# Performance work log

Hardware: AMD Instinct MI355X
Metric: run time of the kernel (lower is better)

The kernel has to match this reference:

```python
import jax, jax.numpy as jnp
import numpy as np

D_NUM, P_NUM, LAYER, EMB = 1500, 4500, 3, 128


def _xavier(k, shape):
    lim = float(np.sqrt(6.0 / (shape[0] + shape[1])))
    return jax.random.uniform(k, shape, minval=-lim, maxval=lim, dtype=jnp.float32)


def _sym_norm(adj):
    # D^{-1/2} A D^{-1/2}, zero-degree safe (utils._create_*_adj_mat)
    deg = adj.sum(axis=1)
    dinv = jnp.where(deg > 0, jax.lax.rsqrt(jnp.maximum(deg, 1e-12)), 0.0)
    return adj * dinv[:, None] * dinv[None, :]


def _gcn(adj, emb, num):
    # LightGCN-style propagation: mean of layer-0..num embeddings (utils._gcn)
    def step(e, _):
        e = adj @ e
        return e, e
    _, layers = jax.lax.scan(step, emb, None, length=num)
    return (emb + layers.sum(axis=0)) / (num + 1)


def _neighbor_mean(mat, feats):
    # vectorized form of the per-row python loop: mean of feats over j where mat[i,j]==1, zeros if no neighbor
    m = (mat == 1.0).astype(feats.dtype)
    cnt = m.sum(axis=1, keepdims=True)
    return jnp.where(cnt > 0, (m @ feats) / jnp.maximum(cnt, 1.0), 0.0)


def _get_weight(emb, WA, BA, HA):
    return jax.nn.log_softmax(jax.nn.relu(emb @ WA + BA) @ HA, axis=0)


def setup_inputs():
    k = jax.random.split(jax.random.key(0), 24)
    N = D_NUM + P_NUM
    A = (jax.random.uniform(k[0], (5, N, N)) < 0.005).astype(jnp.float32)
    z = lambda: jnp.zeros((EMB,), jnp.float32)
    h = lambda: jnp.full((EMB, 1), 0.01, jnp.float32)
    return {
        "A": A,
        "drug_structure": jax.random.normal(k[1], (D_NUM, 160), jnp.float32),
        "protein_structure": jax.random.normal(k[2], (P_NUM, 512), jnp.float32),
        "lin_drug_w": _xavier(k[3], (160, EMB)), "lin_drug_b": z(),
        "lin_pro_w": _xavier(k[4], (512, EMB)), "lin_pro_b": z(),
        "p_weight": _xavier(k[5], (EMB, EMB)),
        "d_weight_i": _xavier(k[6], (EMB, EMB)),
        "pd_weight_p": _xavier(k[7], (EMB, EMB)),
        "pd_weight_d": _xavier(k[8], (EMB, EMB)),
        "dp_weight_p": _xavier(k[9], (EMB, EMB)),
        "WA_drug": _xavier(k[10], (EMB, EMB)), "BA_drug": z(), "HA_drug": h(),
        "WB_drug": _xavier(k[11], (EMB, EMB)), "BB_drug": z(), "HB_drug": h(),
        "WA_pro": _xavier(k[12], (EMB, EMB)), "BA_pro": z(), "HA_pro": h(),
        "WB_pro": _xavier(k[13], (EMB, EMB)), "BB_pro": z(), "HB_pro": h(),
        "WA_sim": _xavier(k[14], (EMB, EMB)), "BA_sim": z(), "HA_sim": h(),
        "layer": LAYER,
    }


def reference(A, drug_structure, protein_structure, lin_drug_w, lin_drug_b, lin_pro_w, lin_pro_b,
              p_weight, d_weight_i, pd_weight_p, pd_weight_d, dp_weight_p,
              WA_drug, BA_drug, HA_drug, WB_drug, BB_drug, HB_drug,
              WA_pro, BA_pro, HA_pro, WB_pro, BB_pro, HB_pro,
              WA_sim, BA_sim, HA_sim, layer):
    D, P = D_NUM, P_NUM
    R = A[0, :D, D:D + P]                       # drug-protein relation [D,P]
    dru_str = drug_structure @ lin_drug_w + lin_drug_b      # [D,128]
    pro_str = protein_structure @ lin_pro_w + lin_pro_b     # [P,128]

    def rel_emb(mat, feats, w):
        nei = _neighbor_mean(mat, feats)
        adj = _sym_norm((mat == 1.0).astype(feats.dtype))
        return _gcn(adj, feats @ w, layer), nei

    dru_rel_emb, dru_rel_nei = rel_emb(A[2, :D, :D], dru_str, d_weight_i)
    pro_rel_emb, pro_rel_nei = rel_emb(A[3, D:, D:], pro_str, p_weight)
    dru_sim_emb, dru_sim_nei = rel_emb(A[4, :D, :D], dru_str, d_weight_i)

    dru_tem = _neighbor_mean(R, pro_rel_nei)    # [D,128]
    # NB: torch 'dru_rel_nei + dru_sim_nei' concatenates python LISTS, and only
    # indices < D are ever read, so pro_tem effectively uses dru_rel_nei only.
    pro_tem = _neighbor_mean(R.T, dru_rel_nei)  # [P,128]

    # bipartite symmetric-normalized adjacency [[0,R],[R^T,0]]
    bip = jnp.zeros((D + P, D + P), R.dtype)
    bip = bip.at[:D, D:].set(R).at[D:, :D].set(R.T)
    adj = _sym_norm(bip)

    one_all = 0.8 * dru_str + 0.2 * dru_tem
    two_all = 0.8 * pro_str + 0.2 * pro_tem
    one_emb = dru_str @ pd_weight_d
    two_all = (two_all @ dp_weight_p) @ pd_weight_d
    two_emb = pro_str @ pd_weight_p
    dru_int = _gcn(adj, jnp.concatenate([one_emb, two_all], axis=0), layer)[:D]
    pro_int = _gcn(adj, jnp.concatenate([one_all, two_emb], axis=0), layer)[D:]

    drug_w = _get_weight(dru_int, WA_drug, BA_drug, HA_drug)
    pro_w = _get_weight(pro_int, WA_pro, BA_pro, HA_pro)
    dru_rel_w = _get_weight(dru_rel_emb, WB_drug, BB_drug, HB_drug)
    pro_rel_w = _get_weight(pro_rel_emb, WB_pro, BB_pro, HB_pro)
    dru_sim_w = _get_weight(dru_sim_emb, WA_sim, BA_sim, HA_sim)

    # faithful to source (including its asymmetric renormalization); dropout is eval-mode identity
    a_w = drug_w / (drug_w + dru_rel_w + dru_sim_w)
    b_w = dru_rel_w / (a_w + dru_rel_w + dru_sim_w)
    c_w = 1.0 - a_w - b_w
    fin_dru = a_w * dru_int + b_w * dru_rel_emb + c_w * dru_sim_emb

    pa = pro_w / (pro_w + pro_rel_w)
    pb = 1.0 - pa
    fin_pro = pa * pro_int + pb * pro_rel_emb

    y = fin_dru @ fin_pro.T                     # [D,P]
    y = (y - y.mean()) / jnp.std(y, ddof=1)     # torch.std is unbiased
    return jax.nn.sigmoid(y)
```

## Files before the change

kernel.cpp:

```cpp
#include <hip/hip_runtime.h>

constexpr int CAP = 128;
constexpr int RS_INV = 1, RS_RSQRT = 2, CS_RSQRT = 4, FINALIZE = 8;

struct BuildSeg { const float* M; long ldm; int rows; int cols; int col_off;
                  int* idx; int* cnt; };
struct LinJob  { const float* X; const float* X2; float pa, pb; int rows; int K;
                 const float* W; const float* bias; float* out; float* out2; };
struct SpmmJob { const int* idx; const int* cnt; int rows; int mod;
                 const float* X; float* out; float* acc; const float* init;
                 float* fin; int flags; };
struct AttnJob { const float* X; int rows; const float* W; const float* B;
                 const float* H; float* s; };

enum { SEG_ZERO = 0, SEG_B0 = 1, SEG_B1, SEG_B2, SEG_B3, SEG_SCAT = 5,
       SEG_SP0 = 6, SEG_SP1 = 7, SEG_LIN0 = 8, SEG_LIN1, SEG_LIN2, SEG_LIN3,
       SEG_AT0 = 12, SEG_AT1, SEG_AT2, SEG_SM0 = 15, SEG_SM1, SEG_SM2,
       NSEG = 18 };

struct Stage {
    int e[NSEG];
    int nZero; int* zeroPtr; double* stats;
    BuildSeg bs[4];
    int scatterTop; int* sIdx; int* sCnt;
    SpmmJob sp[2];
    LinJob lin[4];
    AttnJob at[3];
    float* smv[3]; int smn[3];
};

union SharedU {
    float Ws[32 * 128];
    float red[256];
};


__device__ __forceinline__ void build_unit(const BuildSeg& s, int lb)
{
    int row = lb * 4 + (threadIdx.x >> 6);
    if (row >= s.rows) return;
    int lane = threadIdx.x & 63;
    const float4* p4 = (const float4*)(s.M + (long)row * s.ldm);
    int* ri = s.idx + (long)row * CAP;
    int nv = s.cols >> 2;
    unsigned long long below = (1ULL << lane) - 1ULL;
    if (lane == 63) below = 0x7fffffffffffffffULL;
    int base = 0;
    for (int j0 = 0; j0 < nv; j0 += 64) {
        int jj = j0 + lane;
        float4 v = make_float4(0.f, 0.f, 0.f, 0.f);
        if (jj < nv) v = p4[jj];
        unsigned long long m0 = __ballot(v.x == 1.0f);
        unsigned long long m1 = __ballot(v.y == 1.0f);
        unsigned long long m2 = __ballot(v.z == 1.0f);
        unsigned long long m3 = __ballot(v.w == 1.0f);
        int pre = (int)(__popcll(m0 & below) + __popcll(m1 & below)
                      + __popcll(m2 & below) + __popcll(m3 & below));
        int o = base + pre;
        int cbase = (jj << 2) + s.col_off;
        if (v.x == 1.0f) { if (o < CAP) ri[o] = cbase;     ++o; }
        if (v.y == 1.0f) { if (o < CAP) ri[o] = cbase + 1; ++o; }
        if (v.z == 1.0f) { if (o < CAP) ri[o] = cbase + 2; ++o; }
        if (v.w == 1.0f) { if (o < CAP) ri[o] = cbase + 3; ++o; }
        base += (int)(__popcll(m0) + __popcll(m1) + __popcll(m2) + __popcll(m3));
    }
    if (lane == 0) s.cnt[row] = base < CAP ? base : CAP;
}

__device__ __forceinline__ void scatter_unit(int* idx, int* cnt, int topRows, int lb)
{
    int row = lb * 4 + (threadIdx.x >> 6);
    if (row >= topRows) return;
    int lane = threadIdx.x & 63;
    int n = cnt[row];
    const int* ri = idx + (long)row * CAP;
    for (int k = lane; k < n; k += 64) {
        int j = ri[k];
        int pos = atomicAdd(&cnt[j], 1);
        if (pos < CAP) idx[(long)j * CAP + pos] = row;
    }
}

__device__ __forceinline__ void spmm_tile(const SpmmJob& j, int lb)
{
    int c4 = threadIdx.x & 31;
    int row = lb * 8 + (threadIdx.x >> 5);
    if (row >= j.rows) return;
    int r_loc = row, xoff = 0;
    if (row >= j.mod) { r_loc = row - j.mod; xoff = j.mod; }
    int n = j.cnt[r_loc];
    const int* ri = j.idx + (long)r_loc * CAP;
    const float4* X4 = (const float4*)j.X;
    const bool csq = (j.flags & CS_RSQRT) != 0;
    float ax = 0.f, ay = 0.f, az = 0.f, aw = 0.f;
    int k = 0;
    for (; k + 2 <= n; k += 2) {
        int c0 = ri[k], c1 = ri[k + 1];
        float4 x0 = X4[(long)(c0 + xoff) * 32 + c4];
        float4 x1 = X4[(long)(c1 + xoff) * 32 + c4];
        float s0 = 1.0f, s1 = 1.0f;
        if (csq) {
            int n0 = j.cnt[c0], n1 = j.cnt[c1];
            s0 = (n0 > 0) ? rsqrtf((float)n0) : 0.0f;
            s1 = (n1 > 0) ? rsqrtf((float)n1) : 0.0f;
        }
        ax += x0.x * s0 + x1.x * s1;
        ay += x0.y * s0 + x1.y * s1;
        az += x0.z * s0 + x1.z * s1;
        aw += x0.w * s0 + x1.w * s1;
    }
    if (k < n) {
        int c0 = ri[k];
        float4 x0 = X4[(long)(c0 + xoff) * 32 + c4];
        float s0 = 1.0f;
        if (csq) {
            int n0 = j.cnt[c0];
            s0 = (n0 > 0) ? rsqrtf((float)n0) : 0.0f;
        }
        ax += x0.x * s0; ay += x0.y * s0; az += x0.z * s0; aw += x0.w * s0;
    }
    float rs = 1.0f;
    if (j.flags & RS_INV)        rs = (n > 0) ? 1.0f / (float)n : 0.0f;
    else if (j.flags & RS_RSQRT) rs = (n > 0) ? rsqrtf((float)n) : 0.0f;
    float4 v = make_float4(ax * rs, ay * rs, az * rs, aw * rs);
    long o = (long)row * 32 + c4;
    if (j.flags & FINALIZE) {
        float4 acc = ((const float4*)j.acc)[o];
        ((float4*)j.fin)[o] = make_float4((acc.x + v.x) * 0.25f, (acc.y + v.y) * 0.25f,
                                          (acc.z + v.z) * 0.25f, (acc.w + v.w) * 0.25f);
    } else {
        ((float4*)j.out)[o] = v;
        if (j.acc) {
            float4 base = j.init ? ((const float4*)j.init)[o] : ((const float4*)j.acc)[o];
            ((float4*)j.acc)[o] = make_float4(base.x + v.x, base.y + v.y,
                                              base.z + v.z, base.w + v.w);
        }
    }
}

__device__ void lin_tile(const LinJob& j, int lb, float* Ws)
{
    int c = threadIdx.x & 127;
    int row = lb * 2 + (threadIdx.x >> 7);
    if (j.W == nullptr) {
        if (row < j.rows) {
            long o = (long)row * 128 + c;
            float v = j.pa * j.X[o] + j.pb * j.X2[o];
            j.out[o] = v;
            if (j.out2) j.out2[o] = v;
        }
        return;
    }
    float acc = 0.0f;
    for (int k0 = 0; k0 < j.K; k0 += 32) {
        int chunk = min(32, j.K - k0);
        for (int e = threadIdx.x; e < chunk * 128; e += 256)
            Ws[e] = j.W[(long)(k0 + (e >> 7)) * 128 + (e & 127)];
        __syncthreads();
        if (row < j.rows) {
            const float* xr = j.X + (long)row * j.K + k0;
            const float* x2r = j.X2 ? j.X2 + (long)row * j.K + k0 : nullptr;
            #pragma unroll 4
            for (int kk = 0; kk < chunk; ++kk) {
                float v = xr[kk];
                if (j.X2) v = j.pa * v + j.pb * x2r[kk];
                acc += v * Ws[kk * 128 + c];
            }
        }
        __syncthreads();
    }
    if (row < j.rows) {
        float v = acc + (j.bias ? j.bias[c] : 0.0f);
        j.out[(long)row * 128 + c] = v;
        if (j.out2) j.out2[(long)row * 128 + c] = v;
    }
}

__device__ void attn_tile(const AttnJob& j, int lb, float* Ws)
{
    __shared__ float part[4];
    int c = threadIdx.x & 127;
    int row = lb * 2 + (threadIdx.x >> 7);
    float acc = 0.0f;
    for (int k0 = 0; k0 < 128; k0 += 32) {
        for (int e = threadIdx.x; e < 32 * 128; e += 256)
            Ws[e] = j.W[(long)(k0 + (e >> 7)) * 128 + (e & 127)];
        __syncthreads();
        if (row < j.rows) {
            const float* xr = j.X + (long)row * 128 + k0;
            #pragma unroll 4
            for (int kk = 0; kk < 32; ++kk)
                acc += xr[kk] * Ws[kk * 128 + c];
        }
        __syncthreads();
    }
    float v = 0.0f;
    if (row < j.rows) v = fmaxf(acc + j.B[c], 0.0f) * j.H[c];
    for (int o = 32; o > 0; o >>= 1) v += __shfl_down(v, o, 64);
    if ((threadIdx.x & 63) == 0) part[threadIdx.x >> 6] = v;
    __syncthreads();
    if (threadIdx.x == 0 && row < j.rows)   j.s[row] = part[0] + part[1];
    if (threadIdx.x == 128 && row < j.rows) j.s[row] = part[2] + part[3];
}

__device__ void softmax_vec(float* s, int n, float* red)
{
    int t = threadIdx.x;
    float m = -3.4e38f;
    for (int i = t; i < n; i += 256) m = fmaxf(m, s[i]);
    red[t] = m; __syncthreads();
    for (int o = 128; o > 0; o >>= 1) {
        if (t < o) red[t] = fmaxf(red[t], red[t + o]);
        __syncthreads();
    }
    m = red[0];
    __syncthreads();
    float sum = 0.0f;
    for (int i = t; i < n; i += 256) sum += expf(s[i] - m);
    red[t] = sum; __syncthreads();
    for (int o = 128; o > 0; o >>= 1) {
        if (t < o) red[t] += red[t + o];
        __syncthreads();
    }
    float lse = m + logf(red[0]);
    for (int i = t; i < n; i += 256) s[i] -= lse;
}

__global__ __launch_bounds__(256)
void k_stage(Stage s)
{
    __shared__ SharedU sh;
    int b = blockIdx.x;
    if (b < s.e[SEG_ZERO]) {
        int i = b * 256 + threadIdx.x;
        if (i < s.nZero) s.zeroPtr[i] = 0;
        if (b == 0 && threadIdx.x < 2 && s.stats) s.stats[threadIdx.x] = 0.0;
        return;
    }
    if (b < s.e[SEG_B0]) { build_unit(s.bs[0], b - s.e[SEG_B0 - 1]); return; }
    if (b < s.e[SEG_B1]) { build_unit(s.bs[1], b - s.e[SEG_B1 - 1]); return; }
    if (b < s.e[SEG_B2]) { build_unit(s.bs[2], b - s.e[SEG_B2 - 1]); return; }
    if (b < s.e[SEG_B3]) { build_unit(s.bs[3], b - s.e[SEG_B3 - 1]); return; }
    if (b < s.e[SEG_SCAT]) { scatter_unit(s.sIdx, s.sCnt, s.scatterTop, b - s.e[SEG_SCAT - 1]); return; }
    if (b < s.e[SEG_SP0]) { spmm_tile(s.sp[0], b - s.e[SEG_SP0 - 1]); return; }
    if (b < s.e[SEG_SP1]) { spmm_tile(s.sp[1], b - s.e[SEG_SP1 - 1]); return; }
    if (b < s.e[SEG_LIN0]) { lin_tile(s.lin[0], b - s.e[SEG_LIN0 - 1], sh.Ws); return; }
    if (b < s.e[SEG_LIN1]) { lin_tile(s.lin[1], b - s.e[SEG_LIN1 - 1], sh.Ws); return; }
    if (b < s.e[SEG_LIN2]) { lin_tile(s.lin[2], b - s.e[SEG_LIN2 - 1], sh.Ws); return; }
    if (b < s.e[SEG_LIN3]) { lin_tile(s.lin[3], b - s.e[SEG_LIN3 - 1], sh.Ws); return; }
    if (b < s.e[SEG_AT0]) { attn_tile(s.at[0], b - s.e[SEG_AT0 - 1], sh.Ws); return; }
    if (b < s.e[SEG_AT1]) { attn_tile(s.at[1], b - s.e[SEG_AT1 - 1], sh.Ws); return; }
    if (b < s.e[SEG_AT2]) { attn_tile(s.at[2], b - s.e[SEG_AT2 - 1], sh.Ws); return; }
    if (b < s.e[SEG_SM0]) { softmax_vec(s.smv[0], s.smn[0], sh.red); return; }
    if (b < s.e[SEG_SM1]) { softmax_vec(s.smv[1], s.smn[1], sh.red); return; }
    if (b < s.e[SEG_SM2]) { softmax_vec(s.smv[2], s.smn[2], sh.red); return; }
}

__global__ void k_fin(const float* __restrict__ wd, const float* __restrict__ wdr,
                      const float* __restrict__ wds,
                      const float4* __restrict__ ei, const float4* __restrict__ er,
                      const float4* __restrict__ es,
                      const float* __restrict__ wp, const float* __restrict__ wpr,
                      const float4* __restrict__ pi, const float4* __restrict__ pr,
                      float4* __restrict__ fd, float4* __restrict__ fp,
                      long nD4, long tot4)
{
    long i = (long)blockIdx.x * 256 + threadIdx.x;
    if (i >= tot4) return;
    if (i < nD4) {
        int r = (int)(i >> 5);
        float aL = wd[r], bL = wdr[r], cL = wds[r];
        float x = aL / (aL + bL + cL);
        float y = bL / (x + bL + cL);
        float z = 1.0f - x - y;
        float4 a = ei[i], b = er[i], c = es[i];
        fd[i] = make_float4(x * a.x + y * b.x + z * c.x, x * a.y + y * b.y + z * c.y,
                            x * a.z + y * b.z + z * c.z, x * a.w + y * b.w + z * c.w);
    } else {
        long k = i - nD4;
        int r = (int)(k >> 5);
        float pa = wp[r] / (wp[r] + wpr[r]);
        float pb = 1.0f - pa;
        float4 a = pi[k], b = pr[k];
        fp[k] = make_float4(pa * a.x + pb * b.x, pa * a.y + pb * b.y,
                            pa * a.z + pb * b.z, pa * a.w + pb * b.w);
    }
}

__global__ __launch_bounds__(256)
void k_ygemm(const float* __restrict__ Af, const float* __restrict__ Bf,
             int M, int N, float* __restrict__ y, double* __restrict__ stats)
{
    __shared__ float Ast[32][65];
    __shared__ float Bst[32][65];
    __shared__ double r1[256];
    __shared__ double r2[256];
    int i0 = blockIdx.y * 64, j0 = blockIdx.x * 64;
    int tx = threadIdx.x & 15, ty = threadIdx.x >> 4;
    float acc[4][4] = {};
    for (int k0 = 0; k0 < 128; k0 += 32) {
        for (int e = threadIdx.x; e < 64 * 32; e += 256) {
            int r = e >> 5, kk = e & 31;
            int ia = i0 + r, jb = j0 + r;
            Ast[kk][r] = (ia < M) ? Af[(long)ia * 128 + k0 + kk] : 0.0f;
            Bst[kk][r] = (jb < N) ? Bf[(long)jb * 128 + k0 + kk] : 0.0f;
        }
        __syncthreads();
        #pragma unroll 8
        for (int kk = 0; kk < 32; ++kk) {
            float a0 = Ast[kk][ty];      float a1 = Ast[kk][ty + 16];
            float a2 = Ast[kk][ty + 32]; float a3 = Ast[kk][ty + 48];
            float b0 = Bst[kk][tx];      float b1 = Bst[kk][tx + 16];
            float b2 = Bst[kk][tx + 32]; float b3 = Bst[kk][tx + 48];
            acc[0][0] += a0 * b0; acc[0][1] += a0 * b1; acc[0][2] += a0 * b2; acc[0][3] += a0 * b3;
            acc[1][0] += a1 * b0; acc[1][1] += a1 * b1; acc[1][2] += a1 * b2; acc[1][3] += a1 * b3;
            acc[2][0] += a2 * b0; acc[2][1] += a2 * b1; acc[2][2] += a2 * b2; acc[2][3] += a2 * b3;
            acc[3][0] += a3 * b0; acc[3][1] += a3 * b1; acc[3][2] += a3 * b2; acc[3][3] += a3 * b3;
        }
        __syncthreads();
    }
    double s1 = 0.0, s2 = 0.0;
    #pragma unroll
    for (int q = 0; q < 4; ++q) {
        int i = i0 + ty + 16 * q;
        if (i < M) {
            #pragma unroll
            for (int p = 0; p < 4; ++p) {
                int j = j0 + tx + 16 * p;
                if (j < N) {
                    float v = acc[q][p];
                    y[(long)i * N + j] = v;
                    s1 += v; s2 += (double)v * v;
                }
            }
        }
    }
    r1[threadIdx.x] = s1; r2[threadIdx.x] = s2;
    __syncthreads();
    for (int o = 128; o > 0; o >>= 1) {
        if (threadIdx.x < o) {
            r1[threadIdx.x] += r1[threadIdx.x + o];
            r2[threadIdx.x] += r2[threadIdx.x + o];
        }
        __syncthreads();
    }
    if (threadIdx.x == 0) {
        atomicAdd(&stats[0], r1[0]);
        atomicAdd(&stats[1], r2[0]);
    }
}

__global__ void k_sigmoid(const float* __restrict__ y, const double* __restrict__ stats,
                          long n4, float* __restrict__ out)
{
    long i = (long)blockIdx.x * 256 + threadIdx.x;
    if (i >= n4) return;
    double nd = (double)(n4 * 4);
    double mean = stats[0] / nd;
    double var = (stats[1] - nd * mean * mean) / (nd - 1.0);
    if (var < 1e-30) var = 1e-30;
    float inv = (float)(1.0 / sqrt(var));
    float mu = (float)mean;
    float4 v = ((const float4*)y)[i];
    v.x = 1.0f / (1.0f + expf(-((v.x - mu) * inv)));
    v.y = 1.0f / (1.0f + expf(-((v.y - mu) * inv)));
    v.z = 1.0f / (1.0f + expf(-((v.z - mu) * inv)));
    v.w = 1.0f / (1.0f + expf(-((v.w - mu) * inv)));
    ((float4*)out)[i] = v;
}

extern "C" void kernel_launch(void* const* d_in, const int* in_sizes, int n_in,
                              void* d_out, int out_size, void* d_ws, size_t ws_size,
                              hipStream_t stream)
{
    constexpr int D = 1500, P = 4500, E = 128;
    constexpr int NB = D + P;
    constexpr int NR = D + P + D;
    constexpr long ALD = 6000;
    constexpr long ASZ = 36000000L;

    const float* A    = (const float*)d_in[0];
    const float* drug_structure    = (const float*)d_in[1];
    const float* protein_structure = (const float*)d_in[2];
    const float* lin_drug_w = (const float*)d_in[3];
    const float* lin_drug_b = (const float*)d_in[4];
    const float* lin_pro_w  = (const float*)d_in[5];
    const float* lin_pro_b  = (const float*)d_in[6];
    const float* p_weight   = (const float*)d_in[7];
    const float* d_weight_i = (const float*)d_in[8];
    const float* pd_weight_p = (const float*)d_in[9];
    const float* pd_weight_d = (const float*)d_in[10];
    const float* dp_weight_p = (const float*)d_in[11];
    const float* WA_drug = (const float*)d_in[12];
    const float* BA_drug = (const float*)d_in[13];
    const float* HA_drug = (const float*)d_in[14];
    const float* WB_drug = (const float*)d_in[15];
    const float* BB_drug = (const float*)d_in[16];
    const float* HB_drug = (const float*)d_in[17];
    const float* WA_pro = (const float*)d_in[18];
    const float* BA_pro = (const float*)d_in[19];
    const float* HA_pro = (const float*)d_in[20];
    const float* WB_pro = (const float*)d_in[21];
    const float* BB_pro = (const float*)d_in[22];
    const float* HB_pro = (const float*)d_in[23];
    const float* WA_sim = (const float*)d_in[24];
    const float* BA_sim = (const float*)d_in[25];
    const float* HA_sim = (const float*)d_in[26];

    const float* Rp  = A + 1500;
    const float* A2p = A + 2 * ASZ;
    const float* A3p = A + 3 * ASZ + 1500 * ALD + 1500;
    const float* A4p = A + 4 * ASZ;

    char* wsbase = (char*)d_ws;
    size_t off = 0;
    auto alloc = [&](size_t bytes) -> void* {
        off = (off + 255) & ~(size_t)255;
        void* p = wsbase + off;
        off += bytes;
        return p;
    };
    int*   idx_bip  = (int*)alloc((size_t)NB * CAP * 4);
    int*   cnt_bip  = (int*)alloc((size_t)NB * 4);
    int*   idx_rel  = (int*)alloc((size_t)NR * CAP * 4);
    int*   cnt_rel  = (int*)alloc((size_t)NR * 4);
    float* str_s    = (float*)alloc((size_t)NR * E * 4);
    float* nei_s    = (float*)alloc((size_t)NR * E * 4);
    float* cur_s    = (float*)alloc((size_t)NR * E * 4);
    float* nxt_s    = (float*)alloc((size_t)NR * E * 4);
    float* acc_s    = (float*)alloc((size_t)NR * E * 4);
    float* emb_s    = (float*)alloc((size_t)NR * E * 4);
    float* tem_s    = (float*)alloc((size_t)NB * E * 4);
    float* big_cur  = (float*)alloc((size_t)2 * NB * E * 4);
    float* big_nxt  = (float*)alloc((size_t)2 * NB * E * 4);
    float* big_acc  = (float*)alloc((size_t)2 * NB * E * 4);
    float* int_s    = (float*)alloc((size_t)2 * NB * E * 4);
    float* W2       = (float*)alloc((size_t)E * E * 4);
    float* w_drug = (float*)alloc(D * 4);
    float* w_drel = (float*)alloc(D * 4);
    float* w_dsim = (float*)alloc(D * 4);
    float* w_pro  = (float*)alloc(P * 4);
    float* w_prel = (float*)alloc(P * 4);
    float* fin_dru = (float*)alloc((size_t)D * E * 4);
    float* fin_pro = (float*)alloc((size_t)P * E * 4);
    float* ybuf    = (float*)alloc((size_t)D * P * 4);
    double* stats  = (double*)alloc(2 * sizeof(double));
    (void)ws_size; (void)in_sizes; (void)n_in; (void)out_size;

    float* dru_str = str_s;
    float* pro_str = str_s + (size_t)D * E;
    float* dru_rel_emb = emb_s;
    float* pro_rel_emb = emb_s + (size_t)D * E;
    float* dru_sim_emb = emb_s + (size_t)NB * E;
    float* dru_tem = tem_s;
    float* pro_tem = tem_s + (size_t)D * E;
    float* dru_int = int_s;
    float* pro_int = int_s + (size_t)(NB + D) * E;

    long nD = (long)D * E, nP = (long)P * E;

    auto launch_stage = [&](Stage& s, const int* sz) {
        int tot = 0;
        for (int i = 0; i < NSEG; ++i) { tot += sz[i]; s.e[i] = tot; }
        k_stage<<<tot, 256, 0, stream>>>(s);
    };

    {
        Stage s = {};
        int sz[NSEG] = {};
        sz[SEG_ZERO] = (P + 255) / 256;
        s.nZero = P; s.zeroPtr = cnt_bip + D; s.stats = stats;
        s.bs[0] = { Rp,  ALD, D, P, D,  idx_bip, cnt_bip };                        sz[SEG_B0] = (D + 3) / 4;
        s.bs[1] = { A2p, ALD, D, D, 0,  idx_rel, cnt_rel };                        sz[SEG_B1] = (D + 3) / 4;
        s.bs[2] = { A3p, ALD, P, P, D,  idx_rel + (size_t)D * CAP,  cnt_rel + D }; sz[SEG_B2] = (P + 3) / 4;
        s.bs[3] = { A4p, ALD, D, D, NB, idx_rel + (size_t)NB * CAP, cnt_rel + NB };sz[SEG_B3] = (D + 3) / 4;
        s.lin[0] = { drug_structure, nullptr, 0, 0, D, 160, lin_drug_w, lin_drug_b,
                     dru_str, str_s + (size_t)NB * E };                            sz[SEG_LIN0] = (D + 1) / 2;
        s.lin[1] = { protein_structure, nullptr, 0, 0, P, 512, lin_pro_w, lin_pro_b,
                     pro_str, nullptr };                                           sz[SEG_LIN1] = (P + 1) / 2;
        s.lin[2] = { dp_weight_p, nullptr, 0, 0, E, E, pd_weight_d, nullptr, W2, nullptr };
                                                                                   sz[SEG_LIN2] = (E + 1) / 2;
        launch_stage(s, sz);
    }
    {
        Stage s = {};
        int sz[NSEG] = {};
        s.scatterTop = D; s.sIdx = idx_bip; s.sCnt = cnt_bip;                      sz[SEG_SCAT] = (D + 3) / 4;
        s.sp[0] = { idx_rel, cnt_rel, NR, NR, str_s, nei_s, nullptr, nullptr, nullptr, RS_INV };
                                                                                   sz[SEG_SP0] = (NR + 7) / 8;
        s.lin[0] = { dru_str, nullptr, 0, 0, D, E, d_weight_i, nullptr,
                     cur_s, cur_s + (size_t)NB * E };                              sz[SEG_LIN0] = (D + 1) / 2;
        s.lin[1] = { pro_str, nullptr, 0, 0, P, E, p_weight, nullptr,
                     cur_s + (size_t)D * E, nullptr };                             sz[SEG_LIN1] = (P + 1) / 2;
        launch_stage(s, sz);
    }
    {
        Stage s = {};
        int sz[NSEG] = {};
        s.sp[0] = { idx_rel, cnt_rel, NR, NR, cur_s, nxt_s, acc_s, cur_s, nullptr,
                    RS_RSQRT | CS_RSQRT };                                         sz[SEG_SP0] = (NR + 7) / 8;
        s.sp[1] = { idx_bip, cnt_bip, NB, NB, nei_s, tem_s, nullptr, nullptr, nullptr,
                    RS_INV };                                                      sz[SEG_SP1] = (NB + 7) / 8;
        launch_stage(s, sz);
    }
    {
        Stage s = {};
        int sz[NSEG] = {};
        s.sp[0] = { idx_rel, cnt_rel, NR, NR, nxt_s, cur_s, acc_s, nullptr, nullptr,
                    RS_RSQRT | CS_RSQRT };                                         sz[SEG_SP0] = (NR + 7) / 8;
        s.lin[0] = { dru_str, nullptr, 0, 0, D, E, pd_weight_d, nullptr, big_cur, nullptr };
                                                                                   sz[SEG_LIN0] = (D + 1) / 2;
        s.lin[1] = { pro_str, pro_tem, 0.8f, 0.2f, P, E, W2, nullptr, big_cur + nD, nullptr };
                                                                                   sz[SEG_LIN1] = (P + 1) / 2;
        s.lin[2] = { dru_str, dru_tem, 0.8f, 0.2f, D, E, nullptr, nullptr,
                     big_cur + (size_t)NB * E, nullptr };                          sz[SEG_LIN2] = (D + 1) / 2;
        s.lin[3] = { pro_str, nullptr, 0, 0, P, E, pd_weight_p, nullptr,
                     big_cur + (size_t)(NB + D) * E, nullptr };                    sz[SEG_LIN3] = (P + 1) / 2;
        launch_stage(s, sz);
    }
    {
        Stage s = {};
        int sz[NSEG] = {};
        s.sp[0] = { idx_bip, cnt_bip, 2 * NB, NB, big_cur, big_nxt, big_acc, big_cur,
                    nullptr, RS_RSQRT | CS_RSQRT };                                sz[SEG_SP0] = (2 * NB + 7) / 8;
        s.sp[1] = { idx_rel, cnt_rel, NR, NR, cur_s, nullptr, acc_s, nullptr, emb_s,
                    RS_RSQRT | CS_RSQRT | FINALIZE };                              sz[SEG_SP1] = (NR + 7) / 8;
        launch_stage(s, sz);
    }
    {
        Stage s = {};
        int sz[NSEG] = {};
        s.sp[0] = { idx_bip, cnt_bip, 2 * NB, NB, big_nxt, big_cur, big_acc, nullptr,
                    nullptr, RS_RSQRT | CS_RSQRT };                                sz[SEG_SP0] = (2 * NB + 7) / 8;
        s.at[0] = { dru_rel_emb, D, WB_drug, BB_drug, HB_drug, w_drel };           sz[SEG_AT0] = (D + 1) / 2;
        s.at[1] = { pro_rel_emb, P, WB_pro,  BB_pro,  HB_pro,  w_prel };           sz[SEG_AT1] = (P + 1) / 2;
        s.at[2] = { dru_sim_emb, D, WA_sim,  BA_sim,  HA_sim,  w_dsim };           sz[SEG_AT2] = (D + 1) / 2;
        launch_stage(s, sz);
    }
    {
        Stage s = {};
        int sz[NSEG] = {};
        s.sp[0] = { idx_bip, cnt_bip, 2 * NB, NB, big_cur, nullptr, big_acc, nullptr,
                    int_s, RS_RSQRT | CS_RSQRT | FINALIZE };                       sz[SEG_SP0] = (2 * NB + 7) / 8;
        s.smv[0] = w_drel; s.smn[0] = D;                                           sz[SEG_SM0] = 1;
        s.smv[1] = w_prel; s.smn[1] = P;                                           sz[SEG_SM1] = 1;
        s.smv[2] = w_dsim; s.smn[2] = D;                                           sz[SEG_SM2] = 1;
        launch_stage(s, sz);
    }
    {
        Stage s = {};
        int sz[NSEG] = {};
        s.at[0] = { dru_int, D, WA_drug, BA_drug, HA_drug, w_drug };               sz[SEG_AT0] = (D + 1) / 2;
        s.at[1] = { pro_int, P, WA_pro,  BA_pro,  HA_pro,  w_pro  };               sz[SEG_AT1] = (P + 1) / 2;
        launch_stage(s, sz);
    }
    {
        Stage s = {};
        int sz[NSEG] = {};
        s.smv[0] = w_drug; s.smn[0] = D;                                           sz[SEG_SM0] = 1;
        s.smv[1] = w_pro;  s.smn[1] = P;                                           sz[SEG_SM1] = 1;
        launch_stage(s, sz);
    }
    long nD4 = nD >> 2, tot4 = (nD + nP) >> 2;
    k_fin<<<(int)((tot4 + 255) / 256), 256, 0, stream>>>(
        w_drug, w_drel, w_dsim,
        (const float4*)dru_int, (const float4*)dru_rel_emb, (const float4*)dru_sim_emb,
        w_pro, w_prel, (const float4*)pro_int, (const float4*)pro_rel_emb,
        (float4*)fin_dru, (float4*)fin_pro, nD4, tot4);
    dim3 yg((P + 63) / 64, (D + 63) / 64);
    k_ygemm<<<yg, 256, 0, stream>>>(fin_dru, fin_pro, D, P, ybuf, stats);
    long n4 = ((long)D * P) >> 2;
    k_sigmoid<<<(int)((n4 + 255) / 256), 256, 0, stream>>>(ybuf, stats, n4, (float*)d_out);
}
```

Baseline: 1.307 ms.

## Fuse log-softmax into attention tiles and blend weights into the final GEMM

```diff
diff --git a/kernel.cpp b/kernel.cpp
--- a/kernel.cpp
+++ b/kernel.cpp
@@ -11,22 +11,21 @@
                  const float* X; float* out; float* acc; const float* init;
                  float* fin; int flags; };
 struct AttnJob { const float* X; int rows; const float* W; const float* B;
-                 const float* H; float* s; };
+                 const float* H; float* s; int* ctr; float* lse; int nblk; };
 
 enum { SEG_ZERO = 0, SEG_B0 = 1, SEG_B1, SEG_B2, SEG_B3, SEG_SCAT = 5,
        SEG_SP0 = 6, SEG_SP1 = 7, SEG_LIN0 = 8, SEG_LIN1, SEG_LIN2, SEG_LIN3,
-       SEG_AT0 = 12, SEG_AT1, SEG_AT2, SEG_SM0 = 15, SEG_SM1, SEG_SM2,
-       NSEG = 18 };
+       SEG_AT0 = 12, SEG_AT1, SEG_AT2,
+       NSEG = 15 };
 
 struct Stage {
     int e[NSEG];
-    int nZero; int* zeroPtr; double* stats;
+    int nZero; int* zeroPtr; double* stats; int* actr;
     BuildSeg bs[4];
     int scatterTop; int* sIdx; int* sCnt;
     SpmmJob sp[2];
     LinJob lin[4];
     AttnJob at[3];
-    float* smv[3]; int smn[3];
 };
 
 union SharedU {
@@ -94,22 +93,26 @@
     const bool csq = (j.flags & CS_RSQRT) != 0;
     float ax = 0.f, ay = 0.f, az = 0.f, aw = 0.f;
     int k = 0;
-    for (; k + 2 <= n; k += 2) {
-        int c0 = ri[k], c1 = ri[k + 1];
+    for (; k + 4 <= n; k += 4) {
+        int c0 = ri[k], c1 = ri[k + 1], c2 = ri[k + 2], c3 = ri[k + 3];
         float4 x0 = X4[(long)(c0 + xoff) * 32 + c4];
         float4 x1 = X4[(long)(c1 + xoff) * 32 + c4];
-        float s0 = 1.0f, s1 = 1.0f;
+        float4 x2 = X4[(long)(c2 + xoff) * 32 + c4];
+        float4 x3 = X4[(long)(c3 + xoff) * 32 + c4];
+        float s0 = 1.0f, s1 = 1.0f, s2 = 1.0f, s3 = 1.0f;
         if (csq) {
-            int n0 = j.cnt[c0], n1 = j.cnt[c1];
+            int n0 = j.cnt[c0], n1 = j.cnt[c1], n2 = j.cnt[c2], n3 = j.cnt[c3];
             s0 = (n0 > 0) ? rsqrtf((float)n0) : 0.0f;
             s1 = (n1 > 0) ? rsqrtf((float)n1) : 0.0f;
-        }
-        ax += x0.x * s0 + x1.x * s1;
-        ay += x0.y * s0 + x1.y * s1;
-        az += x0.z * s0 + x1.z * s1;
-        aw += x0.w * s0 + x1.w * s1;
-    }
-    if (k < n) {
+            s2 = (n2 > 0) ? rsqrtf((float)n2) : 0.0f;
+            s3 = (n3 > 0) ? rsqrtf((float)n3) : 0.0f;
+        }
+        ax += (x0.x * s0 + x1.x * s1) + (x2.x * s2 + x3.x * s3);
+        ay += (x0.y * s0 + x1.y * s1) + (x2.y * s2 + x3.y * s3);
+        az += (x0.z * s0 + x1.z * s1) + (x2.z * s2 + x3.z * s3);
+        aw += (x0.w * s0 + x1.w * s1) + (x2.w * s2 + x3.w * s3);
+    }
+    for (; k < n; ++k) {
         int c0 = ri[k];
         float4 x0 = X4[(long)(c0 + xoff) * 32 + c4];
         float s0 = 1.0f;
@@ -176,21 +179,22 @@
     }
 }
 
-__device__ void attn_tile(const AttnJob& j, int lb, float* Ws)
+__device__ void attn_tile(const AttnJob& j, int lb, SharedU& sh)
 {
     __shared__ float part[4];
+    __shared__ int lastFlag;
     int c = threadIdx.x & 127;
     int row = lb * 2 + (threadIdx.x >> 7);
     float acc = 0.0f;
     for (int k0 = 0; k0 < 128; k0 += 32) {
         for (int e = threadIdx.x; e < 32 * 128; e += 256)
-            Ws[e] = j.W[(long)(k0 + (e >> 7)) * 128 + (e & 127)];
+            sh.Ws[e] = j.W[(long)(k0 + (e >> 7)) * 128 + (e & 127)];
         __syncthreads();
         if (row < j.rows) {
             const float* xr = j.X + (long)row * 128 + k0;
             #pragma unroll 4
             for (int kk = 0; kk < 32; ++kk)
-                acc += xr[kk] * Ws[kk * 128 + c];
+                acc += xr[kk] * sh.Ws[kk * 128 + c];
         }
         __syncthreads();
     }
@@ -201,13 +205,17 @@
     __syncthreads();
     if (threadIdx.x == 0 && row < j.rows)   j.s[row] = part[0] + part[1];
     if (threadIdx.x == 128 && row < j.rows) j.s[row] = part[2] + part[3];
-}
-
-__device__ void softmax_vec(float* s, int n, float* red)
-{
-    int t = threadIdx.x;
+    __threadfence();
+    __syncthreads();
+    if (threadIdx.x == 0)
+        lastFlag = (atomicAdd(j.ctr, 1) == j.nblk - 1) ? 1 : 0;
+    __syncthreads();
+    if (!lastFlag) return;
+    __threadfence();
+    int t = threadIdx.x, n = j.rows;
+    float* red = sh.red;
     float m = -3.4e38f;
-    for (int i = t; i < n; i += 256) m = fmaxf(m, s[i]);
+    for (int i = t; i < n; i += 256) m = fmaxf(m, j.s[i]);
     red[t] = m; __syncthreads();
     for (int o = 128; o > 0; o >>= 1) {
         if (t < o) red[t] = fmaxf(red[t], red[t + o]);
@@ -216,14 +224,13 @@
     m = red[0];
     __syncthreads();
     float sum = 0.0f;
-    for (int i = t; i < n; i += 256) sum += expf(s[i] - m);
+    for (int i = t; i < n; i += 256) sum += expf(j.s[i] - m);
     red[t] = sum; __syncthreads();
     for (int o = 128; o > 0; o >>= 1) {
         if (t < o) red[t] += red[t + o];
         __syncthreads();
     }
-    float lse = m + logf(red[0]);
-    for (int i = t; i < n; i += 256) s[i] -= lse;
+    if (t == 0) *j.lse = m + logf(red[0]);
 }
 
 __global__ __launch_bounds__(256)
@@ -235,6 +242,8 @@
         int i = b * 256 + threadIdx.x;
         if (i < s.nZero) s.zeroPtr[i] = 0;
         if (b == 0 && threadIdx.x < 2 && s.stats) s.stats[threadIdx.x] = 0.0;
+        if (b == 0 && threadIdx.x >= 8 && threadIdx.x < 13 && s.actr)
+            s.actr[threadIdx.x - 8] = 0;
         return;
     }
     if (b < s.e[SEG_B0]) { build_unit(s.bs[0], b - s.e[SEG_B0 - 1]); return; }
@@ -248,62 +257,54 @@
     if (b < s.e[SEG_LIN1]) { lin_tile(s.lin[1], b - s.e[SEG_LIN1 - 1], sh.Ws); return; }
     if (b < s.e[SEG_LIN2]) { lin_tile(s.lin[2], b - s.e[SEG_LIN2 - 1], sh.Ws); return; }
     if (b < s.e[SEG_LIN3]) { lin_tile(s.lin[3], b - s.e[SEG_LIN3 - 1], sh.Ws); return; }
-    if (b < s.e[SEG_AT0]) { attn_tile(s.at[0], b - s.e[SEG_AT0 - 1], sh.Ws); return; }
-    if (b < s.e[SEG_AT1]) { attn_tile(s.at[1], b - s.e[SEG_AT1 - 1], sh.Ws); return; }
-    if (b < s.e[SEG_AT2]) { attn_tile(s.at[2], b - s.e[SEG_AT2 - 1], sh.Ws); return; }
-    if (b < s.e[SEG_SM0]) { softmax_vec(s.smv[0], s.smn[0], sh.red); return; }
-    if (b < s.e[SEG_SM1]) { softmax_vec(s.smv[1], s.smn[1], sh.red); return; }
-    if (b < s.e[SEG_SM2]) { softmax_vec(s.smv[2], s.smn[2], sh.red); return; }
-}
-
-__global__ void k_fin(const float* __restrict__ wd, const float* __restrict__ wdr,
-                      const float* __restrict__ wds,
-                      const float4* __restrict__ ei, const float4* __restrict__ er,
-                      const float4* __restrict__ es,
-                      const float* __restrict__ wp, const float* __restrict__ wpr,
-                      const float4* __restrict__ pi, const float4* __restrict__ pr,
-                      float4* __restrict__ fd, float4* __restrict__ fp,
-                      long nD4, long tot4)
-{
-    long i = (long)blockIdx.x * 256 + threadIdx.x;
-    if (i >= tot4) return;
-    if (i < nD4) {
-        int r = (int)(i >> 5);
-        float aL = wd[r], bL = wdr[r], cL = wds[r];
-        float x = aL / (aL + bL + cL);
-        float y = bL / (x + bL + cL);
-        float z = 1.0f - x - y;
-        float4 a = ei[i], b = er[i], c = es[i];
-        fd[i] = make_float4(x * a.x + y * b.x + z * c.x, x * a.y + y * b.y + z * c.y,
-                            x * a.z + y * b.z + z * c.z, x * a.w + y * b.w + z * c.w);
-    } else {
-        long k = i - nD4;
-        int r = (int)(k >> 5);
-        float pa = wp[r] / (wp[r] + wpr[r]);
-        float pb = 1.0f - pa;
-        float4 a = pi[k], b = pr[k];
-        fp[k] = make_float4(pa * a.x + pb * b.x, pa * a.y + pb * b.y,
-                            pa * a.z + pb * b.z, pa * a.w + pb * b.w);
-    }
+    if (b < s.e[SEG_AT0]) { attn_tile(s.at[0], b - s.e[SEG_AT0 - 1], sh); return; }
+    if (b < s.e[SEG_AT1]) { attn_tile(s.at[1], b - s.e[SEG_AT1 - 1], sh); return; }
+    if (b < s.e[SEG_AT2]) { attn_tile(s.at[2], b - s.e[SEG_AT2 - 1], sh); return; }
 }
 
 __global__ __launch_bounds__(256)
-void k_ygemm(const float* __restrict__ Af, const float* __restrict__ Bf,
+void k_ygemm(const float* __restrict__ wdI, const float* __restrict__ wdR,
+             const float* __restrict__ wdS, const float* __restrict__ wpI,
+             const float* __restrict__ wpR, const float* __restrict__ lse,
+             const float* __restrict__ eiI, const float* __restrict__ eiR,
+             const float* __restrict__ eiS,
+             const float* __restrict__ pjI, const float* __restrict__ pjR,
              int M, int N, float* __restrict__ y, double* __restrict__ stats)
 {
     __shared__ float Ast[32][65];
     __shared__ float Bst[32][65];
+    __shared__ float wa[64], wb[64], wc[64], pa[64];
     __shared__ double r1[256];
     __shared__ double r2[256];
     int i0 = blockIdx.y * 64, j0 = blockIdx.x * 64;
+    if (threadIdx.x < 64) {
+        int i = i0 + threadIdx.x;
+        if (i < M) {
+            float aL = wdI[i] - lse[3], bL = wdR[i] - lse[0], cL = wdS[i] - lse[2];
+            float x = aL / (aL + bL + cL);
+            float yv = bL / (x + bL + cL);
+            wa[threadIdx.x] = x; wb[threadIdx.x] = yv; wc[threadIdx.x] = 1.0f - x - yv;
+        }
+    } else if (threadIdx.x < 128) {
+        int j = j0 + (threadIdx.x - 64);
+        if (j < N) {
+            float u = wpI[j] - lse[4], v = wpR[j] - lse[1];
+            pa[threadIdx.x - 64] = u / (u + v);
+        }
+    }
+    __syncthreads();
     int tx = threadIdx.x & 15, ty = threadIdx.x >> 4;
     float acc[4][4] = {};
     for (int k0 = 0; k0 < 128; k0 += 32) {
         for (int e = threadIdx.x; e < 64 * 32; e += 256) {
             int r = e >> 5, kk = e & 31;
             int ia = i0 + r, jb = j0 + r;
-            Ast[kk][r] = (ia < M) ? Af[(long)ia * 128 + k0 + kk] : 0.0f;
-            Bst[kk][r] = (jb < N) ? Bf[(long)jb * 128 + k0 + kk] : 0.0f;
+            long oa = (long)ia * 128 + k0 + kk;
+            long ob = (long)jb * 128 + k0 + kk;
+            Ast[kk][r] = (ia < M)
+                ? wa[r] * eiI[oa] + wb[r] * eiR[oa] + wc[r] * eiS[oa] : 0.0f;
+            Bst[kk][r] = (jb < N)
+                ? pa[r] * pjI[ob] + (1.0f - pa[r]) * pjR[ob] : 0.0f;
         }
         __syncthreads();
         #pragma unroll 8
@@ -441,10 +442,10 @@
     float* w_dsim = (float*)alloc(D * 4);
     float* w_pro  = (float*)alloc(P * 4);
     float* w_prel = (float*)alloc(P * 4);
-    float* fin_dru = (float*)alloc((size_t)D * E * 4);
-    float* fin_pro = (float*)alloc((size_t)P * E * 4);
     float* ybuf    = (float*)alloc((size_t)D * P * 4);
     double* stats  = (double*)alloc(2 * sizeof(double));
+    int*   actr    = (int*)alloc(5 * 4);
+    float* lseArr  = (float*)alloc(5 * 4);
     (void)ws_size; (void)in_sizes; (void)n_in; (void)out_size;
 
     float* dru_str = str_s;
@@ -457,7 +458,7 @@
     float* dru_int = int_s;
     float* pro_int = int_s + (size_t)(NB + D) * E;
 
-    long nD = (long)D * E, nP = (long)P * E;
+    long nD = (long)D * E;
 
     auto launch_stage = [&](Stage& s, const int* sz) {
         int tot = 0;
@@ -469,7 +470,7 @@
         Stage s = {};
         int sz[NSEG] = {};
         sz[SEG_ZERO] = (P + 255) / 256;
-        s.nZero = P; s.zeroPtr = cnt_bip + D; s.stats = stats;
+        s.nZero = P; s.zeroPtr = cnt_bip + D; s.stats = stats; s.actr = actr;
         s.bs[0] = { Rp,  ALD, D, P, D,  idx_bip, cnt_bip };                        sz[SEG_B0] = (D + 3) / 4;
         s.bs[1] = { A2p, ALD, D, D, 0,  idx_rel, cnt_rel };                        sz[SEG_B1] = (D + 3) / 4;
         s.bs[2] = { A3p, ALD, P, P, D,  idx_rel + (size_t)D * CAP,  cnt_rel + D }; sz[SEG_B2] = (P + 3) / 4;
@@ -532,9 +533,12 @@
         int sz[NSEG] = {};
         s.sp[0] = { idx_bip, cnt_bip, 2 * NB, NB, big_nxt, big_cur, big_acc, nullptr,
                     nullptr, RS_RSQRT | CS_RSQRT };                                sz[SEG_SP0] = (2 * NB + 7) / 8;
-        s.at[0] = { dru_rel_emb, D, WB_drug, BB_drug, HB_drug, w_drel };           sz[SEG_AT0] = (D + 1) / 2;
-        s.at[1] = { pro_rel_emb, P, WB_pro,  BB_pro,  HB_pro,  w_prel };           sz[SEG_AT1] = (P + 1) / 2;
-        s.at[2] = { dru_sim_emb, D, WA_sim,  BA_sim,  HA_sim,  w_dsim };           sz[SEG_AT2] = (D + 1) / 2;
+        s.at[0] = { dru_rel_emb, D, WB_drug, BB_drug, HB_drug, w_drel,
+                    actr + 0, lseArr + 0, (D + 1) / 2 };                           sz[SEG_AT0] = (D + 1) / 2;
+        s.at[1] = { pro_rel_emb, P, WB_pro,  BB_pro,  HB_pro,  w_prel,
+                    actr + 1, lseArr + 1, (P + 1) / 2 };                           sz[SEG_AT1] = (P + 1) / 2;
+        s.at[2] = { dru_sim_emb, D, WA_sim,  BA_sim,  HA_sim,  w_dsim,
+                    actr + 2, lseArr + 2, (D + 1) / 2 };                           sz[SEG_AT2] = (D + 1) / 2;
         launch_stage(s, sz);
     }
     {
@@ -542,33 +546,22 @@
         int sz[NSEG] = {};
         s.sp[0] = { idx_bip, cnt_bip, 2 * NB, NB, big_cur, nullptr, big_acc, nullptr,
                     int_s, RS_RSQRT | CS_RSQRT | FINALIZE };                       sz[SEG_SP0] = (2 * NB + 7) / 8;
-        s.smv[0] = w_drel; s.smn[0] = D;                                           sz[SEG_SM0] = 1;
-        s.smv[1] = w_prel; s.smn[1] = P;                                           sz[SEG_SM1] = 1;
-        s.smv[2] = w_dsim; s.smn[2] = D;                                           sz[SEG_SM2] = 1;
-        launch_stage(s, sz);
-    }
-    {
-        Stage s = {};
-        int sz[NSEG] = {};
-        s.at[0] = { dru_int, D, WA_drug, BA_drug, HA_drug, w_drug };               sz[SEG_AT0] = (D + 1) / 2;
-        s.at[1] = { pro_int, P, WA_pro,  BA_pro,  HA_pro,  w_pro  };               sz[SEG_AT1] = (P + 1) / 2;
-        launch_stage(s, sz);
-    }
-    {
-        Stage s = {};
-        int sz[NSEG] = {};
-        s.smv[0] = w_drug; s.smn[0] = D;                                           sz[SEG_SM0] = 1;
-        s.smv[1] = w_pro;  s.smn[1] = P;                                           sz[SEG_SM1] = 1;
-        launch_stage(s, sz);
-    }
-    long nD4 = nD >> 2, tot4 = (nD + nP) >> 2;
-    k_fin<<<(int)((tot4 + 255) / 256), 256, 0, stream>>>(
-        w_drug, w_drel, w_dsim,
-        (const float4*)dru_int, (const float4*)dru_rel_emb, (const float4*)dru_sim_emb,
-        w_pro, w_prel, (const float4*)pro_int, (const float4*)pro_rel_emb,
-        (float4*)fin_dru, (float4*)fin_pro, nD4, tot4);
+        launch_stage(s, sz);
+    }
+    {
+        Stage s = {};
+        int sz[NSEG] = {};
+        s.at[0] = { dru_int, D, WA_drug, BA_drug, HA_drug, w_drug,
+                    actr + 3, lseArr + 3, (D + 1) / 2 };                           sz[SEG_AT0] = (D + 1) / 2;
+        s.at[1] = { pro_int, P, WA_pro,  BA_pro,  HA_pro,  w_pro,
+                    actr + 4, lseArr + 4, (P + 1) / 2 };                           sz[SEG_AT1] = (P + 1) / 2;
+        launch_stage(s, sz);
+    }
     dim3 yg((P + 63) / 64, (D + 63) / 64);
-    k_ygemm<<<yg, 256, 0, stream>>>(fin_dru, fin_pro, D, P, ybuf, stats);
+    k_ygemm<<<yg, 256, 0, stream>>>(w_drug, w_drel, w_dsim, w_pro, w_prel, lseArr,
+                                    dru_int, dru_rel_emb, dru_sim_emb,
+                                    pro_int, pro_rel_emb,
+                                    D, P, ybuf, stats);
     long n4 = ((long)D * P) >> 2;
     k_sigmoid<<<(int)((n4 + 255) / 256), 256, 0, stream>>>(ybuf, stats, n4, (float*)d_out);
 }
```

After: 1.702 ms. +30.2%, slower.
